# Performance work log

Hardware: AMD Instinct MI355X
Metric: run time of the kernel (lower is better)

## Reference

```python
import jax, jax.numpy as jnp
import numpy as np
import math

B, T, C, H = 8, 1024, 1024, 16
D = C // H  # head_size = 64
FF = 4 * C


def setup_inputs() -> dict:
    key = jax.random.key(0)
    ks = jax.random.split(key, 8)
    s = 0.02
    return {
        "x": jax.random.normal(ks[0], (B, T, C), jnp.float32),
        "ln1_g": jnp.ones((C,), jnp.float32),
        "ln1_b": jnp.zeros((C,), jnp.float32),
        "attn_w": jax.random.normal(ks[1], (C, 3 * C), jnp.float32) * s,
        "attn_b": jnp.zeros((3 * C,), jnp.float32),
        "attn_proj_w": jax.random.normal(ks[2], (C, C), jnp.float32) * s,
        "attn_proj_b": jnp.zeros((C,), jnp.float32),
        "ln2_g": jnp.ones((C,), jnp.float32),
        "ln2_b": jnp.zeros((C,), jnp.float32),
        "fc_w": jax.random.normal(ks[3], (C, FF), jnp.float32) * s,
        "fc_b": jnp.zeros((FF,), jnp.float32),
        "mlp_proj_w": jax.random.normal(ks[4], (FF, C), jnp.float32) * s,
        "mlp_proj_b": jnp.zeros((C,), jnp.float32),
    }


def _layernorm(x, g, b, eps=1e-5):
    mu = jnp.mean(x, axis=-1, keepdims=True)
    var = jnp.mean(jnp.square(x - mu), axis=-1, keepdims=True)
    return (x - mu) * jax.lax.rsqrt(var + eps) * g + b


def reference(x, ln1_g, ln1_b, attn_w, attn_b, attn_proj_w, attn_proj_b,
              ln2_g, ln2_b, fc_w, fc_b, mlp_proj_w, mlp_proj_b):
    # --- attention branch (pre-LN) ---
    h = _layernorm(x, ln1_g, ln1_b)
    kqv = h @ attn_w + attn_b                      # (B,T,3C)
    # NOTE: source splits as k, q, v (k first!)
    k, q, v = jnp.split(kqv, 3, axis=-1)
    k = k.reshape(B, T, H, D).transpose(0, 2, 1, 3)  # (B,H,T,D)
    q = q.reshape(B, T, H, D).transpose(0, 2, 1, 3)
    v = v.reshape(B, T, H, D).transpose(0, 2, 1, 3)
    # NOTE: source computes k @ q^T, i.e. wei[i,j] = k_i . q_j
    scale = 1.0 / math.sqrt(D)
    wei = jnp.einsum('bhid,bhjd->bhij', k, q) * scale  # (B,H,T,T)
    causal = jnp.tril(jnp.ones((T, T), dtype=bool))
    wei = jnp.where(causal, wei, -jnp.inf)
    wei = jax.nn.softmax(wei, axis=-1)
    out = jnp.einsum('bhij,bhjd->bhid', wei, v)        # (B,H,T,D)
    out = out.transpose(0, 2, 1, 3).reshape(B, T, C)
    out = out @ attn_proj_w + attn_proj_b
    x = x + out
    # --- MLP branch (pre-LN) ---
    h2 = _layernorm(x, ln2_g, ln2_b)
    m = jax.nn.gelu(h2 @ fc_w + fc_b, approximate=False)  # torch GELU default = exact erf
    m = m @ mlp_proj_w + mlp_proj_b
    return x + m
```

## Files before the change

### kernel.cpp

```cpp
#include <hip/hip_runtime.h>
#include <stdint.h>

typedef unsigned short u16;
typedef __bf16 bf16x8 __attribute__((ext_vector_type(8)));
typedef float f32x4 __attribute__((ext_vector_type(4)));

#define DEVINL static __device__ __forceinline__

DEVINL u16 f2bf(float f) {
  uint32_t u = __builtin_bit_cast(uint32_t, f);
  u += 0x7fffu + ((u >> 16) & 1u);
  return (u16)(u >> 16);
}

DEVINL uint32_t pack_bf2(float f0, float f1) {
  uint32_t u0 = __builtin_bit_cast(uint32_t, f0) + 0x8000u;
  uint32_t u1 = __builtin_bit_cast(uint32_t, f1) + 0x8000u;
  return __builtin_amdgcn_perm(u1, u0, 0x07060302u);
}

DEVINL bf16x8 ld_frag(const u16* p) { return *(const bf16x8*)p; }

DEVINL void gld_lds16(const void* g, void* l) {
  __builtin_amdgcn_global_load_lds((const __attribute__((address_space(1))) void*)g,
                                   (__attribute__((address_space(3))) void*)l, 16, 0, 0);
}

DEVINL int swz4(int r) { return (r & 3) ^ ((r >> 2) & 3); }

DEVINL void xcd_tile(int& tm, int& tn) {
  const int gx = gridDim.x;
  const int flat = blockIdx.x + gx * blockIdx.y;
  const int q = (gx * gridDim.y) >> 3;
  const int wg = (flat & 7) * q + (flat >> 3);
  tn = (wg % gx) * 128;
  tm = (wg / gx) * 128;
}

__global__ __launch_bounds__(256)
void transpose_bf16(const float* __restrict__ W, u16* __restrict__ Wt, int K, int N) {
  __shared__ float tile[32][33];
  const int n0 = blockIdx.x * 32, k0 = blockIdx.y * 32;
  const int tx = threadIdx.x, ty = threadIdx.y;
#pragma unroll
  for (int i = 0; i < 32; i += 8)
    tile[ty + i][tx] = W[(size_t)(k0 + ty + i) * N + n0 + tx];
  __syncthreads();
#pragma unroll
  for (int i = 0; i < 32; i += 8)
    Wt[(size_t)(n0 + ty + i) * K + k0 + tx] = f2bf(tile[tx][ty + i]);
}

__global__ __launch_bounds__(256)
void ln_kernel(const float* __restrict__ x, const float* __restrict__ g,
               const float* __restrict__ b, u16* __restrict__ out) {
  __shared__ float red[8];
  const size_t row = blockIdx.x;
  const int tid = threadIdx.x;
  float4 v = ((const float4*)(x + row * 1024))[tid];
  float s = v.x + v.y + v.z + v.w;
  float s2 = v.x * v.x + v.y * v.y + v.z * v.z + v.w * v.w;
#pragma unroll
  for (int o = 32; o; o >>= 1) { s += __shfl_down(s, o); s2 += __shfl_down(s2, o); }
  const int w = tid >> 6;
  if ((tid & 63) == 0) { red[w * 2] = s; red[w * 2 + 1] = s2; }
  __syncthreads();
  const float S = red[0] + red[2] + red[4] + red[6];
  const float S2 = red[1] + red[3] + red[5] + red[7];
  const float mu = S * (1.f / 1024.f);
  const float var = S2 * (1.f / 1024.f) - mu * mu;
  const float rstd = rsqrtf(var + 1e-5f);
  float4 gv = ((const float4*)g)[tid];
  float4 bv = ((const float4*)b)[tid];
  ushort4 o;
  o.x = f2bf((v.x - mu) * rstd * gv.x + bv.x);
  o.y = f2bf((v.y - mu) * rstd * gv.y + bv.y);
  o.z = f2bf((v.z - mu) * rstd * gv.z + bv.z);
  o.w = f2bf((v.w - mu) * rstd * gv.w + bv.w);
  ((ushort4*)(out + row * 1024))[tid] = o;
}

enum { EPI_KQV = 0, EPI_RESID = 1, EPI_GELU = 2, EPI_ADD = 3 };

template <int EPI>
DEVINL void gemm_epilogue(f32x4 (&acc)[4][4], const float* __restrict__ bias,
                          void* __restrict__ outp, const float* __restrict__ resid,
                          int N, int tm, int tn, int mh, int nh, int q4, int c) {
#pragma unroll
  for (int mt = 0; mt < 4; ++mt) {
#pragma unroll
    for (int nt = 0; nt < 4; ++nt) {
      const int col = tn + nh + nt * 16 + c;
      const float bcol = bias[col];
#pragma unroll
      for (int rg = 0; rg < 4; ++rg) {
        const int row = tm + mh + mt * 16 + q4 * 4 + rg;
        float val = acc[mt][nt][rg] + bcol;
        if constexpr (EPI == EPI_KQV) {
          const int bb = row >> 10, t = row & 1023;
          const int s = col >> 10, rem = col & 1023;
          const int hh = rem >> 6, d = rem & 63;
          if (s == 0) val *= 0.18033688011112042f;
          const size_t base = ((size_t)((bb * 16 + hh) * 3 + s)) << 16;
          const size_t idx = (s == 2) ? base + (size_t)d * 1024 + t : base + (size_t)t * 64 + d;
          ((u16*)outp)[idx] = f2bf(val);
        } else if constexpr (EPI == EPI_RESID) {
          const size_t idx = (size_t)row * 1024 + col;
          ((float*)outp)[idx] = val + resid[idx];
        } else if constexpr (EPI == EPI_GELU) {
          const float x2 = val * val;
          const float t = __builtin_fmaf(x2, -0.102952445f, -2.30221235f);
          const float e = __builtin_amdgcn_exp2f(val * t);
          const float ge = val * __builtin_amdgcn_rcpf(1.0f + e);
          ((u16*)outp)[(size_t)row * N + col] = f2bf(ge);
        } else {
          const size_t idx = (size_t)row * 1024 + col;
          ((float*)outp)[idx] += val;
        }
      }
    }
  }
}

template <int EPI>
DEVINL void gemm_body2(const u16* __restrict__ A, const u16* __restrict__ Bt,
                       const float* __restrict__ bias, void* __restrict__ outp,
                       const float* __restrict__ resid, int M, int N, int K,
                       int tm, int tn) {
  __shared__ alignas(16) u16 sA[2][128 * 32];
  __shared__ alignas(16) u16 sB[2][128 * 32];
  const int tid = threadIdx.x;
  const int w = tid >> 6, l = tid & 63;
  const int q4 = l >> 4, c = l & 15;
  const int mh = (w >> 1) * 64, nh = (w & 1) * 64;
  const int cg8 = (q4 ^ swz4(c)) * 8;

  f32x4 acc[4][4] = {};

  const int srow = l >> 2;
  const int scol = ((l & 3) ^ swz4(srow)) * 8;
  const u16* gA0 = A + (size_t)(tm + (w * 2) * 16 + srow) * K + scol;
  const u16* gA1 = A + (size_t)(tm + (w * 2 + 1) * 16 + srow) * K + scol;
  const u16* gB0 = Bt + (size_t)(tn + (w * 2) * 16 + srow) * K + scol;
  const u16* gB1 = Bt + (size_t)(tn + (w * 2 + 1) * 16 + srow) * K + scol;
  const int cA0 = (w * 2) * 512, cA1 = (w * 2 + 1) * 512;

  const int nIters = K / 32;
#define STAGE2(buf, k0)                         \
  do {                                          \
    gld_lds16(gA0 + (k0), &sA[buf][cA0]);       \
    gld_lds16(gA1 + (k0), &sA[buf][cA1]);       \
    gld_lds16(gB0 + (k0), &sB[buf][cA0]);       \
    gld_lds16(gB1 + (k0), &sB[buf][cA1]);       \
  } while (0)

  STAGE2(0, 0);
  for (int i = 0; i < nIters; ++i) {
    const int cur = i & 1;
    asm volatile("s_waitcnt vmcnt(0)" ::: "memory");
    __syncthreads();
    if (i + 1 < nIters) STAGE2(cur ^ 1, (i + 1) * 32);
    const u16* bA = sA[cur];
    const u16* bB = sB[cur];
    bf16x8 af[4], bfv[4];
#pragma unroll
    for (int mt = 0; mt < 4; ++mt) af[mt] = ld_frag(bA + (mh + mt * 16 + c) * 32 + cg8);
#pragma unroll
    for (int nt = 0; nt < 4; ++nt) bfv[nt] = ld_frag(bB + (nh + nt * 16 + c) * 32 + cg8);
#pragma unroll
    for (int mt = 0; mt < 4; ++mt)
#pragma unroll
      for (int nt = 0; nt < 4; ++nt)
        acc[mt][nt] = __builtin_amdgcn_mfma_f32_16x16x32_bf16(af[mt], bfv[nt], acc[mt][nt], 0, 0, 0);
  }
#undef STAGE2
  gemm_epilogue<EPI>(acc, bias, outp, resid, N, tm, tn, mh, nh, q4, c);
}

template <int EPI>
DEVINL void gemm_bodyW(const u16* __restrict__ A, const u16* __restrict__ Bt,
                       const float* __restrict__ bias, void* __restrict__ outp,
                       const float* __restrict__ resid, int N, int K,
                       int tm, int tn) {
  __shared__ alignas(16) u16 sT[3][48 * 512];
  const int tid = threadIdx.x;
  const int w = tid >> 6, l = tid & 63;
  const int q4 = l >> 4, c = l & 15;
  const int mh = (w >> 1) * 64, nh = (w & 1) * 64;

  f32x4 acc[4][4] = {};

  const int lr = l >> 3;
  const int lc = ((l & 7) ^ lr) * 8;
  const u16* gA[4];
  const u16* gB[2];
#pragma unroll
  for (int j = 0; j < 4; ++j) gA[j] = A + (size_t)(tm + 32 * w + j * 8 + lr) * K + lc;
#pragma unroll
  for (int j = 0; j < 2; ++j) gB[j] = Bt + (size_t)(tn + 16 * w + j * 8 + lr) * K + lc;

  auto stageW = [&](int buf, int k0) {
#pragma unroll
    for (int j = 0; j < 4; ++j) gld_lds16(gA[j] + k0, &sT[buf][(4 * w + j) * 512]);
#pragma unroll
    for (int j = 0; j < 2; ++j) gld_lds16(gB[j] + k0, &sT[buf][(32 + 2 * w + j) * 512]);
  };

  auto computeW = [&](int cur) {
    const u16* bufA = sT[cur];
    const u16* bufB = sT[cur] + 32 * 512;
#pragma unroll
    for (int kh = 0; kh < 2; ++kh) {
      bf16x8 af[4], bfv[4];
#pragma unroll
      for (int mt = 0; mt < 4; ++mt) {
        const int row = mh + mt * 16 + c;
        af[mt] = ld_frag(bufA + row * 64 + ((kh * 4 + q4) ^ (c & 7)) * 8);
      }
#pragma unroll
      for (int nt = 0; nt < 4; ++nt) {
        const int row = nh + nt * 16 + c;
        bfv[nt] = ld_frag(bufB + row * 64 + ((kh * 4 + q4) ^ (c & 7)) * 8);
      }
      __builtin_amdgcn_s_setprio(1);
#pragma unroll
      for (int mt = 0; mt < 4; ++mt)
#pragma unroll
        for (int nt = 0; nt < 4; ++nt)
          acc[mt][nt] = __builtin_amdgcn_mfma_f32_16x16x32_bf16(af[mt], bfv[nt], acc[mt][nt], 0, 0, 0);
      __builtin_amdgcn_s_setprio(0);
    }
  };

  const int nI = K / 64;
  stageW(0, 0);
  stageW(1, 64);
  int bc = 0;
  int i = 0;
  for (; i < nI - 1; ++i) {
    asm volatile("s_waitcnt vmcnt(6)" ::: "memory");
    __builtin_amdgcn_s_barrier();
    asm volatile("" ::: "memory");
    if (i + 2 < nI) {
      const int tgt = (bc >= 1) ? bc - 1 : 2;
      stageW(tgt, (i + 2) * 64);
    }
    computeW(bc);
    bc = (bc < 2) ? bc + 1 : 0;
  }
  asm volatile("s_waitcnt vmcnt(0)" ::: "memory");
  __builtin_amdgcn_s_barrier();
  asm volatile("" ::: "memory");
  computeW(bc);

  gemm_epilogue<EPI>(acc, bias, outp, resid, N, tm, tn, mh, nh, q4, c);
}

__global__ __launch_bounds__(256)
void gemm_kqv(const u16* __restrict__ A, const u16* __restrict__ Bt,
              const float* __restrict__ bias, u16* __restrict__ outp,
              int M, int N, int K) {
  int tm, tn;
  xcd_tile(tm, tn);
  gemm_body2<EPI_KQV>(A, Bt, bias, outp, nullptr, M, N, K, tm, tn);
}

__global__ __launch_bounds__(256)
void gemm_gelu(const u16* __restrict__ A, const u16* __restrict__ Bt,
               const float* __restrict__ bias, u16* __restrict__ outp,
               int M, int N, int K) {
  int tm, tn;
  xcd_tile(tm, tn);
  gemm_body2<EPI_GELU>(A, Bt, bias, outp, nullptr, M, N, K, tm, tn);
}

DEVINL void xcd_tile_wide(int& tm, int& tn) {
  const int flat = blockIdx.x + 8 * blockIdx.y;
  const int wg = (flat & 7) * 32 + (flat >> 3);
  tn = (wg & 7) * 128;
  tm = (wg >> 3) * 256;
}

__global__ __launch_bounds__(512)
void gemm_resid(const u16* __restrict__ A, const u16* __restrict__ Bt,
                const float* __restrict__ bias, float* __restrict__ outp,
                const float* __restrict__ resid, int M, int N, int K) {
  int tm, tn;
  xcd_tile_wide(tm, tn);
  gemm_bodyW<EPI_RESID>(A, Bt, bias, outp, resid, N, K, tm, tn);
}

__global__ __launch_bounds__(512)
void gemm_add(const u16* __restrict__ A, const u16* __restrict__ Bt,
              const float* __restrict__ bias, float* __restrict__ outp,
              int M, int N, int K) {
  int tm, tn;
  xcd_tile_wide(tm, tn);
  gemm_bodyW<EPI_ADD>(A, Bt, bias, outp, nullptr, N, K, tm, tn);
}

__global__ __launch_bounds__(256)
void attn_kernel(const u16* __restrict__ kqv, u16* __restrict__ outp) {
  constexpr int LS = 72;
  __shared__ alignas(16) u16 sP[64 * LS];
  __shared__ alignas(16) u16 sK[64 * LS];
  __shared__ alignas(16) u16 sV[64 * LS];
  const int bh = blockIdx.x;
  const int it = (int)gridDim.y - 1 - (int)blockIdx.y;
  const int tid = threadIdx.x;
  const int w = tid >> 6, l = tid & 63, q4 = l >> 4, c = l & 15;
  const int il = w * 16 + c;
  const size_t hb = (size_t)bh * 3 * 65536;
  const u16* qbase = kqv + hb;
  const u16* kbase = kqv + hb + 65536;
  const u16* vbase = kqv + hb + 2 * 65536;

  const int sr = tid >> 3, sc = (tid & 7) * 8;
  const int sr2 = sr + 32;
  *(int4*)&sP[sr * LS + sc] = *(const int4*)(qbase + (size_t)(it * 64 + sr) * 64 + sc);
  *(int4*)&sP[sr2 * LS + sc] = *(const int4*)(qbase + (size_t)(it * 64 + sr2) * 64 + sc);

  f32x4 oacc[4] = {};
  float lsum = 0.f;
  bf16x8 bq0, bq1;

  for (int jt = 0; jt <= it; ++jt) {
    if (jt) __syncthreads();
    *(int4*)&sK[sr * LS + sc] = *(const int4*)(kbase + (size_t)(jt * 64 + sr) * 64 + sc);
    *(int4*)&sK[sr2 * LS + sc] = *(const int4*)(kbase + (size_t)(jt * 64 + sr2) * 64 + sc);
    *(int4*)&sV[sr * LS + sc] = *(const int4*)(vbase + (size_t)sr * 1024 + jt * 64 + sc);
    *(int4*)&sV[sr2 * LS + sc] = *(const int4*)(vbase + (size_t)sr2 * 1024 + jt * 64 + sc);
    __syncthreads();
    if (jt == 0) {
      bq0 = ld_frag(sP + il * LS + q4 * 8);
      bq1 = ld_frag(sP + il * LS + 32 + q4 * 8);
    }

    f32x4 st[4] = {};
#pragma unroll
    for (int nt = 0; nt < 4; ++nt) {
      st[nt] = __builtin_amdgcn_mfma_f32_16x16x32_bf16(
          ld_frag(sK + (nt * 16 + c) * LS + q4 * 8), bq0, st[nt], 0, 0, 0);
      st[nt] = __builtin_amdgcn_mfma_f32_16x16x32_bf16(
          ld_frag(sK + (nt * 16 + c) * LS + 32 + q4 * 8), bq1, st[nt], 0, 0, 0);
    }

    const bool diag = (jt == it);
    u16* prow = sP + il * LS;
#pragma unroll
    for (int nt = 0; nt < 4; ++nt) {
      float e0 = __builtin_amdgcn_exp2f(st[nt][0]);
      float e1 = __builtin_amdgcn_exp2f(st[nt][1]);
      float e2 = __builtin_amdgcn_exp2f(st[nt][2]);
      float e3 = __builtin_amdgcn_exp2f(st[nt][3]);
      if (diag) {
        const int jb = nt * 16 + q4 * 4;
        e0 = (jb + 0 > il) ? 0.f : e0;
        e1 = (jb + 1 > il) ? 0.f : e1;
        e2 = (jb + 2 > il) ? 0.f : e2;
        e3 = (jb + 3 > il) ? 0.f : e3;
      }
      lsum += (e0 + e1) + (e2 + e3);
      uint2 pk = {pack_bf2(e0, e1), pack_bf2(e2, e3)};
      *(uint2*)&prow[nt * 16 + q4 * 4] = pk;
    }

    bf16x8 bp0 = ld_frag(sP + il * LS + q4 * 8);
    bf16x8 bp1 = ld_frag(sP + il * LS + 32 + q4 * 8);
#pragma unroll
    for (int dt = 0; dt < 4; ++dt) {
      oacc[dt] = __builtin_amdgcn_mfma_f32_16x16x32_bf16(
          ld_frag(sV + (dt * 16 + c) * LS + q4 * 8), bp0, oacc[dt], 0, 0, 0);
      oacc[dt] = __builtin_amdgcn_mfma_f32_16x16x32_bf16(
          ld_frag(sV + (dt * 16 + c) * LS + 32 + q4 * 8), bp1, oacc[dt], 0, 0, 0);
    }
  }

  lsum += __shfl_xor(lsum, 16);
  lsum += __shfl_xor(lsum, 32);
  const float linv = 1.f / lsum;

  const int b_ = bh >> 4, h_ = bh & 15;
  const int t_ = it * 64 + il;
  u16* orow = outp + ((size_t)(b_ * 1024 + t_)) * 1024 + h_ * 64;
#pragma unroll
  for (int dt = 0; dt < 4; ++dt) {
    uint2 ok = {pack_bf2(oacc[dt][0] * linv, oacc[dt][1] * linv),
                pack_bf2(oacc[dt][2] * linv, oacc[dt][3] * linv)};
    *(uint2*)&orow[dt * 16 + q4 * 4] = ok;
  }
}

extern "C" void kernel_launch(void* const* d_in, const int* in_sizes, int n_in,
                              void* d_out, int out_size, void* d_ws, size_t ws_size,
                              hipStream_t stream) {
  const float* x       = (const float*)d_in[0];
  const float* ln1_g   = (const float*)d_in[1];
  const float* ln1_b   = (const float*)d_in[2];
  const float* attn_w  = (const float*)d_in[3];
  const float* attn_b  = (const float*)d_in[4];
  const float* attn_pw = (const float*)d_in[5];
  const float* attn_pb = (const float*)d_in[6];
  const float* ln2_g   = (const float*)d_in[7];
  const float* ln2_b   = (const float*)d_in[8];
  const float* fc_w    = (const float*)d_in[9];
  const float* fc_b    = (const float*)d_in[10];
  const float* mlp_w   = (const float*)d_in[11];
  const float* mlp_b   = (const float*)d_in[12];
  float* out = (float*)d_out;

  u16* ws = (u16*)d_ws;
  u16* mlpT     = ws;
  u16* attn_wT  = mlpT + 1024 * 4096;
  u16* attn_pwT = attn_wT + 3072 * 1024;
  u16* fcT      = attn_pwT + 1024 * 1024;
  u16* hbuf     = fcT + 4096 * 1024;
  u16* kqv      = hbuf + 8192 * 1024;
  u16* attn_o   = kqv + (size_t)8192 * 3072;
  u16* mbuf     = kqv;

  dim3 tb(32, 8);
  transpose_bf16<<<dim3(96, 32),  tb, 0, stream>>>(attn_w,  attn_wT,  1024, 3072);
  transpose_bf16<<<dim3(32, 32),  tb, 0, stream>>>(attn_pw, attn_pwT, 1024, 1024);
  transpose_bf16<<<dim3(128, 32), tb, 0, stream>>>(fc_w,    fcT,      1024, 4096);
  transpose_bf16<<<dim3(32, 128), tb, 0, stream>>>(mlp_w,   mlpT,     4096, 1024);

  ln_kernel<<<8192, 256, 0, stream>>>(x, ln1_g, ln1_b, hbuf);

  gemm_kqv<<<dim3(24, 64), 256, 0, stream>>>(hbuf, attn_wT, attn_b, kqv, 8192, 3072, 1024);

  attn_kernel<<<dim3(128, 16), 256, 0, stream>>>(kqv, attn_o);

  gemm_resid<<<dim3(8, 32), 512, 0, stream>>>(attn_o, attn_pwT, attn_pb, out, x,
                                              8192, 1024, 1024);

  ln_kernel<<<8192, 256, 0, stream>>>(out, ln2_g, ln2_b, hbuf);

  gemm_gelu<<<dim3(32, 64), 256, 0, stream>>>(hbuf, fcT, fc_b, mbuf, 8192, 4096, 1024);

  gemm_add<<<dim3(8, 32), 512, 0, stream>>>(mbuf, mlpT, mlp_b, out, 8192, 1024, 4096);
}
```

Before: 464.9 us.

## Use wide 256x128 GEMM body for GELU and register-prefetch K/V tiles in attention

The FC+GELU GEMM switches from the 128x128 256-thread body to the wide 256x128 512-thread body, with a generalized XCD-aware tile mapping, so each block gets more reuse of its B tile. The attention kernel now loads the next K/V tile from global memory into registers while the current tile is being computed. This hides global load latency behind the MFMA work. The cost is higher register pressure in attention and a grid with half as many GEMM blocks.

```diff
diff --git a/kernel.cpp b/kernel.cpp
--- a/kernel.cpp
+++ b/kernel.cpp
@@ -35,6 +35,15 @@
   const int wg = (flat & 7) * q + (flat >> 3);
   tn = (wg % gx) * 128;
   tm = (wg / gx) * 128;
+}
+
+DEVINL void xcd_tile_wide(int& tm, int& tn) {
+  const int gx = gridDim.x;
+  const int flat = blockIdx.x + gx * blockIdx.y;
+  const int q = (gx * gridDim.y) >> 3;
+  const int wg = (flat & 7) * q + (flat >> 3);
+  tn = (wg % gx) * 128;
+  tm = (wg / gx) * 256;
 }
 
 __global__ __launch_bounds__(256)
@@ -265,20 +274,13 @@
   gemm_body2<EPI_KQV>(A, Bt, bias, outp, nullptr, M, N, K, tm, tn);
 }
 
-__global__ __launch_bounds__(256)
+__global__ __launch_bounds__(512)
 void gemm_gelu(const u16* __restrict__ A, const u16* __restrict__ Bt,
                const float* __restrict__ bias, u16* __restrict__ outp,
                int M, int N, int K) {
   int tm, tn;
-  xcd_tile(tm, tn);
-  gemm_body2<EPI_GELU>(A, Bt, bias, outp, nullptr, M, N, K, tm, tn);
-}
-
-DEVINL void xcd_tile_wide(int& tm, int& tn) {
-  const int flat = blockIdx.x + 8 * blockIdx.y;
-  const int wg = (flat & 7) * 32 + (flat >> 3);
-  tn = (wg & 7) * 128;
-  tm = (wg >> 3) * 256;
+  xcd_tile_wide(tm, tn);
+  gemm_bodyW<EPI_GELU>(A, Bt, bias, outp, nullptr, N, K, tm, tn);
 }
 
 __global__ __launch_bounds__(512)
@@ -324,13 +326,24 @@
   float lsum = 0.f;
   bf16x8 bq0, bq1;
 
+  int4 rk0 = *(const int4*)(kbase + (size_t)sr * 64 + sc);
+  int4 rk1 = *(const int4*)(kbase + (size_t)sr2 * 64 + sc);
+  int4 rv0 = *(const int4*)(vbase + (size_t)sr * 1024 + sc);
+  int4 rv1 = *(const int4*)(vbase + (size_t)sr2 * 1024 + sc);
+
   for (int jt = 0; jt <= it; ++jt) {
     if (jt) __syncthreads();
-    *(int4*)&sK[sr * LS + sc] = *(const int4*)(kbase + (size_t)(jt * 64 + sr) * 64 + sc);
-    *(int4*)&sK[sr2 * LS + sc] = *(const int4*)(kbase + (size_t)(jt * 64 + sr2) * 64 + sc);
-    *(int4*)&sV[sr * LS + sc] = *(const int4*)(vbase + (size_t)sr * 1024 + jt * 64 + sc);
-    *(int4*)&sV[sr2 * LS + sc] = *(const int4*)(vbase + (size_t)sr2 * 1024 + jt * 64 + sc);
+    *(int4*)&sK[sr * LS + sc] = rk0;
+    *(int4*)&sK[sr2 * LS + sc] = rk1;
+    *(int4*)&sV[sr * LS + sc] = rv0;
+    *(int4*)&sV[sr2 * LS + sc] = rv1;
     __syncthreads();
+    if (jt < it) {
+      rk0 = *(const int4*)(kbase + (size_t)((jt + 1) * 64 + sr) * 64 + sc);
+      rk1 = *(const int4*)(kbase + (size_t)((jt + 1) * 64 + sr2) * 64 + sc);
+      rv0 = *(const int4*)(vbase + (size_t)sr * 1024 + (jt + 1) * 64 + sc);
+      rv1 = *(const int4*)(vbase + (size_t)sr2 * 1024 + (jt + 1) * 64 + sc);
+    }
     if (jt == 0) {
       bq0 = ld_frag(sP + il * LS + q4 * 8);
       bq1 = ld_frag(sP + il * LS + 32 + q4 * 8);
@@ -436,7 +449,7 @@
 
   ln_kernel<<<8192, 256, 0, stream>>>(out, ln2_g, ln2_b, hbuf);
 
-  gemm_gelu<<<dim3(32, 64), 256, 0, stream>>>(hbuf, fcT, fc_b, mbuf, 8192, 4096, 1024);
+  gemm_gelu<<<dim3(32, 32), 512, 0, stream>>>(hbuf, fcT, fc_b, mbuf, 8192, 4096, 1024);
 
   gemm_add<<<dim3(8, 32), 512, 0, stream>>>(mbuf, mlpT, mlp_b, out, 8192, 1024, 4096);
 }
```

Result: no change. 468.0 us (+0.7%).
